# Kernel optimization log

Measured on AMD Instinct MI355X. Metric: run time of the kernel, lower is better.

Reference implementation:

```python
import jax, jax.numpy as jnp
import numpy as np

C = 51  # num_relation


def setup_inputs() -> dict:
    key = jax.random.key(0)
    N_o, N_u, D = 16384, 16384, 1024
    k = jax.random.split(key, 6)
    feat = jax.random.normal(k[0], (N_o + N_u, D), jnp.float32)
    # first N_o rows are labeled (label != 0), remaining N_u rows unlabeled (label == 0)
    label = jnp.concatenate([
        jax.random.randint(k[1], (N_o,), 1, C),
        jnp.zeros((N_u,), jnp.int32),
    ]).astype(jnp.int32)
    W_o = jax.random.normal(k[2], (C, D), jnp.float32) * 0.03
    b_o = jnp.zeros((C,), jnp.float32)
    W = jax.random.normal(k[3], (C, D), jnp.float32) * 0.03
    b = jnp.zeros((C,), jnp.float32)
    cls = jnp.arange(C)
    group_mid_mask = (cls >= 16) & (cls < 36)   # groups[1]
    group_tail_mask = cls >= 36                 # groups[2]
    # runtime torch.randint partner sampling, hoisted to input construction
    idx_m = jax.random.randint(k[4], (2, N_u), 0, N_o)  # 2 mid copies
    idx_t = jax.random.randint(k[5], (3, N_u), 0, N_o)  # 3 tail copies
    return dict(feat=feat, label=label, W_o=W_o, b_o=b_o, W=W, b=b,
                group_mid_mask=group_mid_mask, group_tail_mask=group_tail_mask,
                idx_m=idx_m, idx_t=idx_t)


def reference(feat, label, W_o, b_o, W, b, group_mid_mask, group_tail_mask, idx_m, idx_t):
    n_u = idx_m.shape[1]
    n_o = feat.shape[0] - n_u
    feat_o, feat_u = feat[:n_o], feat[n_o:]
    label_o = label[:n_o]

    # fc_o under no_grad, then softmax / top-1 rank + score
    logits = jax.lax.stop_gradient(feat_u @ W_o.T + b_o)      # [N_u, C]
    p = jax.nn.softmax(logits, axis=1)
    pred = jnp.argmax(p, axis=1)                               # ranks[:,0]
    score = jnp.max(p, axis=1)                                 # score[:,0]

    # group membership + confidence thresholds (heads are unused in the original)
    mid_m = group_mid_mask[pred] & (score > 0.5)
    tail_m = group_tail_mask[pred] & (score > 0.3)

    oh_u = jax.nn.one_hot(pred, C, dtype=feat.dtype)
    oh_o = jax.nn.one_hot(label_o, C, dtype=feat.dtype)

    im = idx_m.reshape(-1)   # [2*N_u]
    it = idx_t.reshape(-1)   # [3*N_u]

    fm = 0.7 * feat_o[im] + 0.3 * jnp.tile(feat_u, (2, 1))
    lm = 0.7 * oh_o[im] + 0.3 * jnp.tile(oh_u, (2, 1))
    ft = 0.7 * feat_o[it] + 0.3 * jnp.tile(feat_u, (3, 1))
    lt = 0.7 * oh_o[it] + 0.3 * jnp.tile(oh_u, (3, 1))

    feat_cat = jnp.concatenate([fm, ft], axis=0)               # [5*N_u, D]
    label_cat = jnp.concatenate([lm, lt], axis=0)              # [5*N_u, C]
    w = jnp.concatenate([jnp.tile(mid_m, 2), jnp.tile(tail_m, 3)]).astype(feat.dtype)

    # soft-label cross entropy on fc(feat_cat); masked mean over selected rows
    logp = jax.nn.log_softmax(feat_cat @ W.T + b, axis=1)
    ce = -(logp * label_cat).sum(axis=1)
    cnt = w.sum()
    return (ce * w).sum() / jnp.maximum(cnt, 1.0)
```

## Files before the change

### kernel.cpp

```cpp
#include <hip/hip_runtime.h>
#include <math.h>

#define DD 1024
#define NU 16384
#define NO 16384

typedef short short8 __attribute__((ext_vector_type(8)));
typedef float f32x4 __attribute__((ext_vector_type(4)));

__device__ __forceinline__ unsigned short f2b(float x) {
    unsigned int u = __float_as_uint(x);
    u += 0x7FFFu + ((u >> 16) & 1u);
    return (unsigned short)(u >> 16);
}

__device__ __forceinline__ short8 cvt8(float4 a, float4 b) {
    short8 r;
    r[0] = (short)f2b(a.x); r[1] = (short)f2b(a.y);
    r[2] = (short)f2b(a.z); r[3] = (short)f2b(a.w);
    r[4] = (short)f2b(b.x); r[5] = (short)f2b(b.y);
    r[6] = (short)f2b(b.z); r[7] = (short)f2b(b.w);
    return r;
}

__device__ __forceinline__ void gl_lds(const void* g, void* l) {
    __builtin_amdgcn_global_load_lds(
        (const __attribute__((address_space(1))) void*)g,
        (__attribute__((address_space(3))) void*)l, 16, 0, 0);
}

__global__ __launch_bounds__(256) void fused(const float* __restrict__ feat,
                                             const float* __restrict__ W_o,
                                             const float* __restrict__ b_o,
                                             const float* __restrict__ W,
                                             const float* __restrict__ bb,
                                             const int* __restrict__ label,
                                             const int* __restrict__ idxm,
                                             const int* __restrict__ idxt,
                                             double* __restrict__ pnum,
                                             int* __restrict__ pcnt) {
    __shared__ __attribute__((aligned(16))) char lds[3 * 16384];
    __shared__ int2 slist[192];
    __shared__ int scount;
    __shared__ float swsum[4];
    __shared__ int swcnt[4];

    const int m0 = blockIdx.x * 64;
    const int tid = threadIdx.x;
    const int lane = tid & 63;
    const int w = tid >> 6;
    const int m = lane & 15;
    const int quad = lane >> 4;
    const int s = m & 7;

    if (tid == 0) scount = 0;
    __syncthreads();

    const char *gs0, *gs1, *gs2, *gs3;
    int lo0, lo1, lo2, lo3;
    { const int r = w * 16 + (lane >> 3);
      const int g = (lane & 7) ^ (r & 7);
      gs0 = (const char*)(feat + (size_t)(NO + m0 + r) * DD + g * 4); lo0 = (w * 2) * 1024; }
    { const int r = w * 16 + 8 + (lane >> 3);
      const int g = (lane & 7) ^ (r & 7);
      gs1 = (const char*)(feat + (size_t)(NO + m0 + r) * DD + g * 4); lo1 = (w * 2 + 1) * 1024; }
    { const int r = w * 16 + (lane >> 3);
      const int rc = (r > 50) ? 50 : r;
      const int g = (lane & 7) ^ (r & 7);
      gs2 = (const char*)(W_o + (size_t)rc * DD + g * 4); lo2 = 8192 + (w * 2) * 1024; }
    { const int r = w * 16 + 8 + (lane >> 3);
      const int rc = (r > 50) ? 50 : r;
      const int g = (lane & 7) ^ (r & 7);
      gs3 = (const char*)(W_o + (size_t)rc * DD + g * 4); lo3 = 8192 + (w * 2 + 1) * 1024; }

    f32x4 acc[4];
#pragma unroll
    for (int nf = 0; nf < 4; ++nf) acc[nf] = (f32x4){0.f, 0.f, 0.f, 0.f};

    const int rA = w * 16 + m;

#define STAGE(t, buf)                                  \
    do {                                               \
        gl_lds(gs0 + (size_t)(t) * 128, (buf) + lo0);  \
        gl_lds(gs1 + (size_t)(t) * 128, (buf) + lo1);  \
        gl_lds(gs2 + (size_t)(t) * 128, (buf) + lo2);  \
        gl_lds(gs3 + (size_t)(t) * 128, (buf) + lo3);  \
    } while (0)

    STAGE(0, lds);
    STAGE(1, lds + 16384);

    int bc = 0;
    for (int kt = 0; kt < 32; ++kt) {
        if (kt < 30) {
            const int bi2 = (bc == 0) ? 2 : bc - 1;
            STAGE(kt + 2, lds + bi2 * 16384);
            asm volatile("s_waitcnt vmcnt(8)\n\ts_barrier" ::: "memory");
        } else if (kt == 30) {
            asm volatile("s_waitcnt vmcnt(4)\n\ts_barrier" ::: "memory");
        } else {
            asm volatile("s_waitcnt vmcnt(0)\n\ts_barrier" ::: "memory");
        }
        const char* buf = lds + bc * 16384;
        const float4 f0 = *(const float4*)(buf + rA * 128 + ((2 * quad) ^ s) * 16);
        const float4 f1 = *(const float4*)(buf + rA * 128 + ((2 * quad + 1) ^ s) * 16);
        const short8 af = cvt8(f0, f1);
#pragma unroll
        for (int nf = 0; nf < 4; ++nf) {
            const int row = m + nf * 16;
            const float4 b0 = *(const float4*)(buf + 8192 + row * 128 + ((2 * quad) ^ s) * 16);
            const float4 b1 = *(const float4*)(buf + 8192 + row * 128 + ((2 * quad + 1) ^ s) * 16);
            const short8 bf = cvt8(b0, b1);
            acc[nf] = __builtin_amdgcn_mfma_f32_16x16x32_bf16(af, bf, acc[nf], 0, 0, 0);
        }
        bc = (bc == 2) ? 0 : bc + 1;
    }
#undef STAGE

    const int rloc = m0 + w * 16 + quad * 4;
    float boc[4];
#pragma unroll
    for (int c = 0; c < 4; ++c) {
        const int col = c * 16 + m;
        boc[c] = (col < 51) ? b_o[col] : 0.f;
    }
#pragma unroll
    for (int r = 0; r < 4; ++r) {
        float z[4];
        float mx = acc[0][r] + boc[0];
        int mi = m;
        z[0] = mx;
#pragma unroll
        for (int c = 1; c < 4; ++c) {
            const int col = c * 16 + m;
            z[c] = (col < 51) ? acc[c][r] + boc[c] : -INFINITY;
            if (z[c] > mx) { mx = z[c]; mi = col; }
        }
#pragma unroll
        for (int off = 1; off < 16; off <<= 1) {
            const float om = __shfl_xor(mx, off);
            const int oi = __shfl_xor(mi, off);
            if (om > mx || (om == mx && oi < mi)) { mx = om; mi = oi; }
        }
        float e = 0.f;
#pragma unroll
        for (int c = 0; c < 4; ++c)
            if (c * 16 + m < 51) e += expf(z[c] - mx);
#pragma unroll
        for (int off = 1; off < 16; off <<= 1) e += __shfl_xor(e, off);
        const float score = 1.f / e;
        const int mid = (mi >= 16 && mi < 36 && score > 0.5f) ? 1 : 0;
        const int tail = (mi >= 36 && score > 0.3f) ? 1 : 0;
        const int nref = mid ? 2 : (tail ? 3 : 0);
        if (m < nref) {
            const int u = rloc + r;
            const int oo = mid ? idxm[(size_t)m * NU + u]
                               : idxt[(size_t)m * NU + u];
            const int p = atomicAdd(&scount, 1);
            slist[p] = make_int2(oo, u | (mi << 16));
        }
    }
    __syncthreads();

    const int n = scount;
    const float bbv = (lane < 51) ? bb[lane] : 0.f;
    float fsum = 0.f;
    int ccnt = 0;
    for (int t = w; t < n; t += 4) {
        const int2 e = slist[t];
        const int ob = e.x;
        const int ub = e.y & 0xFFFF;
        const int pu = e.y >> 16;
        const f32x4* fo4 = (const f32x4*)(feat + (size_t)ob * DD);
        const f32x4* fu4 = (const f32x4*)(feat + (size_t)(NO + ub) * DD);
        f32x4 g[4];
#pragma unroll
        for (int q = 0; q < 4; ++q)
            g[q] = 0.7f * fo4[q * 64 + lane] + 0.3f * fu4[q * 64 + lane];
        float zmy = 0.f;
        for (int c = 0; c < 51; ++c) {
            const f32x4* wr = (const f32x4*)(W + (size_t)c * DD);
            f32x4 p = wr[lane] * g[0];
            p += wr[64 + lane] * g[1];
            p += wr[128 + lane] * g[2];
            p += wr[192 + lane] * g[3];
            float d = (p[0] + p[1]) + (p[2] + p[3]);
#pragma unroll
            for (int off = 1; off < 64; off <<= 1) d += __shfl_xor(d, off);
            if (lane == c) zmy = d;
        }
        const float z = (lane < 51) ? zmy + bbv : -INFINITY;
        float mx = z;
#pragma unroll
        for (int off = 1; off < 64; off <<= 1) mx = fmaxf(mx, __shfl_xor(mx, off));
        float e2 = (lane < 51) ? expf(z - mx) : 0.f;
#pragma unroll
        for (int off = 1; off < 64; off <<= 1) e2 += __shfl_xor(e2, off);
        const float lse = mx + logf(e2);
        const int lo = label[ob];
        const float zlo = __shfl(z, lo);
        const float zpu = __shfl(z, pu);
        fsum += lse - 0.7f * zlo - 0.3f * zpu;
        ++ccnt;
    }
    if (lane == 0) { swsum[w] = fsum; swcnt[w] = ccnt; }
    __syncthreads();
    if (tid == 0) {
        pnum[blockIdx.x] = (double)swsum[0] + (double)swsum[1] +
                           (double)swsum[2] + (double)swsum[3];
        pcnt[blockIdx.x] = swcnt[0] + swcnt[1] + swcnt[2] + swcnt[3];
    }
}

__global__ __launch_bounds__(256) void finalize(const double* __restrict__ pnum,
                                                const int* __restrict__ pcnt,
                                                float* __restrict__ out) {
    __shared__ double sd[4];
    __shared__ int sc[4];
    const int w = threadIdx.x >> 6;
    const int lane = threadIdx.x & 63;
    double s = pnum[threadIdx.x];
    int c = pcnt[threadIdx.x];
#pragma unroll
    for (int off = 1; off < 64; off <<= 1) {
        s += __shfl_xor(s, off);
        c += __shfl_xor(c, off);
    }
    if (lane == 0) { sd[w] = s; sc[w] = c; }
    __syncthreads();
    if (threadIdx.x == 0) {
        const double n = sd[0] + sd[1] + sd[2] + sd[3];
        const int cc = sc[0] + sc[1] + sc[2] + sc[3];
        out[0] = (float)(n / (cc > 1 ? (double)cc : 1.0));
    }
}

extern "C" void kernel_launch(void* const* d_in, const int* in_sizes, int n_in,
                              void* d_out, int out_size, void* d_ws, size_t ws_size,
                              hipStream_t stream) {
    const float* feat = (const float*)d_in[0];
    const int* label = (const int*)d_in[1];
    const float* W_o = (const float*)d_in[2];
    const float* b_o = (const float*)d_in[3];
    const float* W = (const float*)d_in[4];
    const float* b = (const float*)d_in[5];
    const int* idxm = (const int*)d_in[8];
    const int* idxt = (const int*)d_in[9];

    char* ws = (char*)d_ws;
    double* pnum = (double*)ws;
    int* pcnt = (int*)(ws + 2048);

    fused<<<256, 256, 0, stream>>>(feat, W_o, b_o, W, b, label, idxm, idxt,
                                   pnum, pcnt);
    finalize<<<1, 256, 0, stream>>>(pnum, pcnt, (float*)d_out);
}
```

Before: 226.4 us.

## Preconvert W_o to bf16 in LDS and stream A rows through registers

```diff
diff --git a/kernel.cpp b/kernel.cpp
--- a/kernel.cpp
+++ b/kernel.cpp
@@ -21,12 +21,6 @@
     r[4] = (short)f2b(b.x); r[5] = (short)f2b(b.y);
     r[6] = (short)f2b(b.z); r[7] = (short)f2b(b.w);
     return r;
-}
-
-__device__ __forceinline__ void gl_lds(const void* g, void* l) {
-    __builtin_amdgcn_global_load_lds(
-        (const __attribute__((address_space(1))) void*)g,
-        (__attribute__((address_space(3))) void*)l, 16, 0, 0);
 }
 
 __global__ __launch_bounds__(256) void fused(const float* __restrict__ feat,
@@ -39,85 +33,77 @@
                                              const int* __restrict__ idxt,
                                              double* __restrict__ pnum,
                                              int* __restrict__ pcnt) {
-    __shared__ __attribute__((aligned(16))) char lds[3 * 16384];
+    __shared__ __attribute__((aligned(16))) unsigned short Bs[32][64][32];
     __shared__ int2 slist[192];
     __shared__ int scount;
     __shared__ float swsum[4];
     __shared__ int swcnt[4];
 
-    const int m0 = blockIdx.x * 64;
     const int tid = threadIdx.x;
     const int lane = tid & 63;
     const int w = tid >> 6;
     const int m = lane & 15;
     const int quad = lane >> 4;
-    const int s = m & 7;
 
     if (tid == 0) scount = 0;
-    __syncthreads();
-
-    const char *gs0, *gs1, *gs2, *gs3;
-    int lo0, lo1, lo2, lo3;
-    { const int r = w * 16 + (lane >> 3);
-      const int g = (lane & 7) ^ (r & 7);
-      gs0 = (const char*)(feat + (size_t)(NO + m0 + r) * DD + g * 4); lo0 = (w * 2) * 1024; }
-    { const int r = w * 16 + 8 + (lane >> 3);
-      const int g = (lane & 7) ^ (r & 7);
-      gs1 = (const char*)(feat + (size_t)(NO + m0 + r) * DD + g * 4); lo1 = (w * 2 + 1) * 1024; }
-    { const int r = w * 16 + (lane >> 3);
-      const int rc = (r > 50) ? 50 : r;
-      const int g = (lane & 7) ^ (r & 7);
-      gs2 = (const char*)(W_o + (size_t)rc * DD + g * 4); lo2 = 8192 + (w * 2) * 1024; }
-    { const int r = w * 16 + 8 + (lane >> 3);
-      const int rc = (r > 50) ? 50 : r;
-      const int g = (lane & 7) ^ (r & 7);
-      gs3 = (const char*)(W_o + (size_t)rc * DD + g * 4); lo3 = 8192 + (w * 2 + 1) * 1024; }
+
+#pragma unroll 8
+    for (int i = tid; i < 51 * 256; i += 256) {
+        const int row = i >> 8;
+        const int c = i & 255;
+        const int k0 = c * 4;
+        const int kt = k0 >> 5;
+        const int kl = k0 & 31;
+        const int c4 = kl >> 3;
+        const int half = (kl >> 2) & 1;
+        const float4 v = *(const float4*)(W_o + (size_t)row * DD + k0);
+        ushort4 o;
+        o.x = f2b(v.x); o.y = f2b(v.y); o.z = f2b(v.z); o.w = f2b(v.w);
+        char* dst = (char*)&Bs[kt][row][0] + ((c4 ^ (row & 3)) * 16 + half * 8);
+        *(ushort4*)dst = o;
+    }
+#pragma unroll 4
+    for (int i = tid; i < 13 * 256; i += 256) {
+        const int row = 51 + (i >> 8);
+        const int j = i & 255;
+        char* dst = (char*)&Bs[j >> 3][row][0] + (j & 7) * 8;
+        *(ushort4*)dst = make_ushort4(0, 0, 0, 0);
+    }
+    __syncthreads();
+
+    const int urow = blockIdx.x * 64 + w * 16 + m;
+    const char* abase = (const char*)(feat + (size_t)(NO + urow) * DD) + quad * 32;
+    const int bswz = (quad ^ (m & 3)) * 16;
 
     f32x4 acc[4];
 #pragma unroll
     for (int nf = 0; nf < 4; ++nf) acc[nf] = (f32x4){0.f, 0.f, 0.f, 0.f};
 
-    const int rA = w * 16 + m;
-
-#define STAGE(t, buf)                                  \
-    do {                                               \
-        gl_lds(gs0 + (size_t)(t) * 128, (buf) + lo0);  \
-        gl_lds(gs1 + (size_t)(t) * 128, (buf) + lo1);  \
-        gl_lds(gs2 + (size_t)(t) * 128, (buf) + lo2);  \
-        gl_lds(gs3 + (size_t)(t) * 128, (buf) + lo3);  \
-    } while (0)
-
-    STAGE(0, lds);
-    STAGE(1, lds + 16384);
-
-    int bc = 0;
+    float4 pa0[8], pa1[8];
+#pragma unroll
+    for (int t = 0; t < 8; ++t) {
+        pa0[t] = *(const float4*)(abase + (size_t)t * 128);
+        pa1[t] = *(const float4*)(abase + (size_t)t * 128 + 16);
+    }
+#pragma unroll
     for (int kt = 0; kt < 32; ++kt) {
-        if (kt < 30) {
-            const int bi2 = (bc == 0) ? 2 : bc - 1;
-            STAGE(kt + 2, lds + bi2 * 16384);
-            asm volatile("s_waitcnt vmcnt(8)\n\ts_barrier" ::: "memory");
-        } else if (kt == 30) {
-            asm volatile("s_waitcnt vmcnt(4)\n\ts_barrier" ::: "memory");
-        } else {
-            asm volatile("s_waitcnt vmcnt(0)\n\ts_barrier" ::: "memory");
-        }
-        const char* buf = lds + bc * 16384;
-        const float4 f0 = *(const float4*)(buf + rA * 128 + ((2 * quad) ^ s) * 16);
-        const float4 f1 = *(const float4*)(buf + rA * 128 + ((2 * quad + 1) ^ s) * 16);
+        const int slot = kt & 7;
+        const float4 f0 = pa0[slot];
+        const float4 f1 = pa1[slot];
+        if (kt < 24) {
+            pa0[slot] = *(const float4*)(abase + (size_t)(kt + 8) * 128);
+            pa1[slot] = *(const float4*)(abase + (size_t)(kt + 8) * 128 + 16);
+        }
         const short8 af = cvt8(f0, f1);
 #pragma unroll
         for (int nf = 0; nf < 4; ++nf) {
-            const int row = m + nf * 16;
-            const float4 b0 = *(const float4*)(buf + 8192 + row * 128 + ((2 * quad) ^ s) * 16);
-            const float4 b1 = *(const float4*)(buf + 8192 + row * 128 + ((2 * quad + 1) ^ s) * 16);
-            const short8 bf = cvt8(b0, b1);
+            const short8 bf =
+                *(const short8*)((const char*)&Bs[kt][m + nf * 16][0] + bswz);
             acc[nf] = __builtin_amdgcn_mfma_f32_16x16x32_bf16(af, bf, acc[nf], 0, 0, 0);
         }
-        bc = (bc == 2) ? 0 : bc + 1;
-    }
-#undef STAGE
-
-    const int rloc = m0 + w * 16 + quad * 4;
+    }
+
+    const int rloc = blockIdx.x * 64 + w * 16 + quad * 4;
     float boc[4];
 #pragma unroll
     for (int c = 0; c < 4; ++c) {
```

Result: no change. 222.8 us (-1.6%).
